# Performance work log

Hardware: AMD Instinct MI355X
Metric: run time of the kernel (lower is better)

The kernel has to match this reference:

```python
import jax, jax.numpy as jnp
import numpy as np

N, E = 40000, 640000
NODE_DIM, EDGE_DIM, H = 128, 64, 8
DK = NODE_DIM // H


def setup_inputs() -> dict:
    key = jax.random.key(0)
    ks = jax.random.split(key, 12)
    s = 1.0 / np.sqrt(NODE_DIM)
    se = 1.0 / np.sqrt(EDGE_DIM)
    return {
        "nodes": jax.random.normal(ks[0], (N, NODE_DIM), jnp.float32),
        "edge_index": jax.random.randint(ks[1], (2, E), 0, N, jnp.int64),
        "edge_attr": jax.random.normal(ks[2], (E, EDGE_DIM), jnp.float32),
        # Linear weights stored as [in, out] so y = x @ W + b
        "wq": jax.random.uniform(ks[3], (NODE_DIM, NODE_DIM), jnp.float32, -s, s),
        "bq": jnp.zeros((NODE_DIM,), jnp.float32),
        "wk": jax.random.uniform(ks[4], (NODE_DIM, NODE_DIM), jnp.float32, -s, s),
        "bk": jnp.zeros((NODE_DIM,), jnp.float32),
        "wv": jax.random.uniform(ks[5], (NODE_DIM, NODE_DIM), jnp.float32, -s, s),
        "bv": jnp.zeros((NODE_DIM,), jnp.float32),
        "we": jax.random.uniform(ks[6], (EDGE_DIM, NODE_DIM), jnp.float32, -se, se),
        "be": jnp.zeros((NODE_DIM,), jnp.float32),
        "wo": jax.random.uniform(ks[7], (NODE_DIM, NODE_DIM), jnp.float32, -s, s),
        "bo": jnp.zeros((NODE_DIM,), jnp.float32),
    }


def reference(nodes, edge_index, edge_attr, wq, bq, wk, bk, wv, bv, we, be, wo, bo):
    n = nodes.shape[0]
    inv_sqrt_dk = 1.0 / np.sqrt(DK).astype(np.float32)
    Q = (nodes @ wq + bq).reshape(n, H, DK)
    K = (nodes @ wk + bk).reshape(n, H, DK)
    V = (nodes @ wv + bv).reshape(n, H, DK)
    row, col = edge_index[0], edge_index[1]
    Qr = Q[row]                                   # [E, H, DK]
    scores = (Qr * K[col]).sum(-1) * inv_sqrt_dk  # [E, H]
    ef = (edge_attr @ we + be).reshape(-1, H, DK)
    scores = scores + (Qr * ef).sum(-1) * inv_sqrt_dk
    es = jnp.exp(scores)                          # unnormalized exp (matches torch code: no max-subtraction)
    denom = jax.ops.segment_sum(es, row, num_segments=n)       # [N, H]
    w = es / (denom[row] + 1e-8)                  # [E, H]
    msg = w[..., None] * V[col]                   # [E, H, DK]
    out = jax.ops.segment_sum(msg, row, num_segments=n).reshape(n, -1)
    return out @ wo + bo
```

## Files before the change

kernel.cpp:

```cpp
#include <hip/hip_runtime.h>
#include <hip/hip_fp16.h>

#define NN  40000
#define NE  640000
#define ND  128
#define ED  64
#define NH  8
#define DK  16
#define NWT 912

#define SCAN_NBLK 157
#define PREP_NBLK 524
#define GEMM1_NBLK 625

typedef _Float16 f16x8 __attribute__((ext_vector_type(8)));
typedef float    f32x4 __attribute__((ext_vector_type(4)));

__global__ __launch_bounds__(256) void k_prep_hist(const float* __restrict__ wq,
                                                   const float* __restrict__ bq,
                                                   const float* __restrict__ wk,
                                                   const float* __restrict__ bk,
                                                   const float* __restrict__ wv,
                                                   const float* __restrict__ bv,
                                                   const float* __restrict__ we,
                                                   const float* __restrict__ be,
                                                   const float* __restrict__ wo,
                                                   const int* __restrict__ ei,
                                                   __half* __restrict__ WT,
                                                   __half* __restrict__ woT,
                                                   float* __restrict__ bias_all,
                                                   int* __restrict__ hist) {
  if (blockIdx.x >= PREP_NBLK) {
    const int e = (blockIdx.x - PREP_NBLK) * 256 + threadIdx.x;
    if (e < NE) atomicAdd(&hist[ei[e]], 1);
    return;
  }
  int idx = blockIdx.x * 256 + threadIdx.x;
  if (idx < NWT * ND) {
    const int n = idx >> 7, k = idx & 127;
    float v;
    if (n < 128)      v = wq[k * ND + n];
    else if (n < 256) v = wk[k * ND + (n - 128)];
    else if (n < 384) v = wv[k * ND + (n - 256)];
    else if (n < 896) {
      const int col = n - 384, h = col >> 6, j = col & 63;
      const float4* a = (const float4*)(wq + (size_t)k * ND + h * DK);
      const float4* b = (const float4*)(we + (size_t)j * ND + h * DK);
      float s = 0.f;
#pragma unroll
      for (int i = 0; i < 4; ++i) {
        float4 av = a[i], bv4 = b[i];
        s = fmaf(av.x, bv4.x, s); s = fmaf(av.y, bv4.y, s);
        s = fmaf(av.z, bv4.z, s); s = fmaf(av.w, bv4.w, s);
      }
      v = 0.25f * s;
    } else if (n < 904) {
      const int h = n - 896;
      const float4* a = (const float4*)(wq + (size_t)k * ND + h * DK);
      const float4* b = (const float4*)(be + h * DK);
      float s = 0.f;
#pragma unroll
      for (int i = 0; i < 4; ++i) {
        float4 av = a[i], bv4 = b[i];
        s = fmaf(av.x, bv4.x, s); s = fmaf(av.y, bv4.y, s);
        s = fmaf(av.z, bv4.z, s); s = fmaf(av.w, bv4.w, s);
      }
      v = 0.25f * s;
    } else v = 0.f;
    WT[idx] = __float2half_rn(v);
    return;
  }
  idx -= NWT * ND;
  if (idx < ND * ND) {
    const int n = idx >> 7, k = idx & 127;
    woT[idx] = __float2half_rn(wo[k * ND + n]);
    return;
  }
  idx -= ND * ND;
  if (idx < NWT) {
    float v;
    if (idx < 128)      v = bq[idx];
    else if (idx < 256) v = bk[idx - 128];
    else if (idx < 384) v = bv[idx - 256];
    else if (idx < 896) {
      const int col = idx - 384, h = col >> 6, j = col & 63;
      const float4* a = (const float4*)(bq + h * DK);
      const float4* b = (const float4*)(we + (size_t)j * ND + h * DK);
      float s = 0.f;
#pragma unroll
      for (int i = 0; i < 4; ++i) {
        float4 av = a[i], bv4 = b[i];
        s = fmaf(av.x, bv4.x, s); s = fmaf(av.y, bv4.y, s);
        s = fmaf(av.z, bv4.z, s); s = fmaf(av.w, bv4.w, s);
      }
      v = 0.25f * s;
    } else if (idx < 904) {
      const int h = idx - 896;
      const float4* a = (const float4*)(bq + h * DK);
      const float4* b = (const float4*)(be + h * DK);
      float s = 0.f;
#pragma unroll
      for (int i = 0; i < 4; ++i) {
        float4 av = a[i], bv4 = b[i];
        s = fmaf(av.x, bv4.x, s); s = fmaf(av.y, bv4.y, s);
        s = fmaf(av.z, bv4.z, s); s = fmaf(av.w, bv4.w, s);
      }
      v = 0.25f * s;
    } else v = 0.f;
    bias_all[idx] = v;
  }
}

__global__ __launch_bounds__(256) void k_gemm1_scatter(const float* __restrict__ x,
                                                       const __half* __restrict__ WT,
                                                       const float* __restrict__ bias_all,
                                                       const int* __restrict__ ei,
                                                       int* __restrict__ cursor,
                                                       int2* __restrict__ pair,
                                                       __half* __restrict__ qh,
                                                       __half* __restrict__ K16,
                                                       __half* __restrict__ V16,
                                                       __half* __restrict__ G16,
                                                       float* __restrict__ SB) {
  __shared__ _Float16 bs[4][16][132];

  if (blockIdx.x >= GEMM1_NBLK) {
    const int e = (blockIdx.x - GEMM1_NBLK) * 256 + threadIdx.x;
    if (e < NE) {
      const int row = ei[e];
      const int col = ei[NE + e];
      const int pos = atomicAdd(&cursor[row], 1);
      pair[pos] = make_int2(col, e);
    }
    return;
  }

  const int wave = threadIdx.x >> 6;
  const int l    = threadIdx.x & 63;
  const int row  = l & 15;
  const int kq   = l >> 4;
  const int r0   = blockIdx.x * 64 + wave * 16;

  f16x8 a[4];
#pragma unroll
  for (int s = 0; s < 4; ++s) {
    const float4* ap = (const float4*)(x + (size_t)(r0 + row) * ND + s * 32 + kq * 8);
    const float4 f0 = ap[0], f1 = ap[1];
    f16x8 t;
    t[0] = (_Float16)f0.x; t[1] = (_Float16)f0.y; t[2] = (_Float16)f0.z; t[3] = (_Float16)f0.w;
    t[4] = (_Float16)f1.x; t[5] = (_Float16)f1.y; t[6] = (_Float16)f1.z; t[7] = (_Float16)f1.w;
    a[s] = t;
  }

  const int rb = r0 + kq * 4;

  for (int nc = 0; nc < 56; nc += 4) {
    __syncthreads();
    {
      const __half* src = WT + (size_t)((nc + wave) * 16 + row) * ND;
      _Float16* dst = &bs[wave][row][0];
#pragma unroll
      for (int ch = 0; ch < 4; ++ch) {
        const int o = (kq + ch * 4) * 8;
        *(f16x8*)(dst + o) = *(const f16x8*)(src + o);
      }
    }
    __syncthreads();
#pragma unroll
    for (int t = 0; t < 4; ++t) {
      const int nt = nc + t;
      f32x4 c = {0.f, 0.f, 0.f, 0.f};
#pragma unroll
      for (int s = 0; s < 4; ++s) {
        const f16x8 b = *(const f16x8*)&bs[t][row][s * 32 + kq * 8];
        c = __builtin_amdgcn_mfma_f32_16x16x32_f16(a[s], b, c, 0, 0, 0);
      }
      const int col = nt * 16 + row;
      const float bb = bias_all[col];
      if (nt < 24) {
        __half* dst = (nt < 8) ? (qh + col) : (nt < 16) ? (K16 + (col - 128)) : (V16 + (col - 256));
#pragma unroll
        for (int i = 0; i < 4; ++i)
          dst[(size_t)(rb + i) * ND] = __float2half_rn(c[i] + bb);
      } else {
        const int gcol = col - 384;
#pragma unroll
        for (int i = 0; i < 4; ++i)
          G16[(size_t)(rb + i) * 512 + gcol] = __float2half_rn(c[i] + bb);
      }
    }
  }

  {
    f32x4 c = {0.f, 0.f, 0.f, 0.f};
#pragma unroll
    for (int s = 0; s < 4; ++s) {
      const f16x8 b = *(const f16x8*)(WT + (size_t)(896 + row) * ND + s * 32 + kq * 8);
      c = __builtin_amdgcn_mfma_f32_16x16x32_f16(a[s], b, c, 0, 0, 0);
    }
    if (row < 8) {
      const float bb = bias_all[896 + row];
#pragma unroll
      for (int i = 0; i < 4; ++i)
        SB[(size_t)(rb + i) * NH + row] = c[i] + bb;
    }
  }
}

__global__ __launch_bounds__(256) void k_gemm2(const __half* __restrict__ mh,
                                               const __half* __restrict__ woT,
                                               const float* __restrict__ bo,
                                               float* __restrict__ out) {
  __shared__ _Float16 ws[128][132];
  const int tid  = threadIdx.x;
  const int wave = tid >> 6;
  const int l    = tid & 63;
  const int row  = l & 15;
  const int kq   = l >> 4;
  const int r0   = blockIdx.x * 64 + wave * 16;

  {
    const int r = tid & 127, hf = tid >> 7;
    const __half* src = woT + (size_t)r * ND + hf * 64;
    _Float16* dst = &ws[r][hf * 64];
#pragma unroll
    for (int ch = 0; ch < 8; ++ch)
      *(f16x8*)(dst + ch * 8) = *(const f16x8*)(src + ch * 8);
  }

  f16x8 a[4];
#pragma unroll
  for (int s = 0; s < 4; ++s)
    a[s] = *(const f16x8*)(mh + (size_t)(r0 + row) * ND + s * 32 + kq * 8);

  __syncthreads();

  const int rb = r0 + kq * 4;
#pragma unroll 2
  for (int nt = 0; nt < 8; ++nt) {
    f32x4 c = {0.f, 0.f, 0.f, 0.f};
#pragma unroll
    for (int s = 0; s < 4; ++s) {
      const f16x8 b = *(const f16x8*)&ws[nt * 16 + row][s * 32 + kq * 8];
      c = __builtin_amdgcn_mfma_f32_16x16x32_f16(a[s], b, c, 0, 0, 0);
    }
    const int col = nt * 16 + row;
    const float bb = bo[col];
#pragma unroll
    for (int i = 0; i < 4; ++i)
      out[(size_t)(rb + i) * ND + col] = c[i] + bb;
  }
}

__global__ __launch_bounds__(256) void k_scan1(const int* __restrict__ hist,
                                               int* __restrict__ off,
                                               int* __restrict__ bsum) {
  __shared__ int sh[256];
  const int tid = threadIdx.x;
  const int idx = blockIdx.x * 256 + tid;
  int v = (idx < NN) ? hist[idx] : 0;
  sh[tid] = v;
  __syncthreads();
#pragma unroll
  for (int d = 1; d < 256; d <<= 1) {
    int t = (tid >= d) ? sh[tid - d] : 0;
    __syncthreads();
    sh[tid] += t;
    __syncthreads();
  }
  if (idx < NN) off[idx] = sh[tid] - v;
  if (tid == 255) bsum[blockIdx.x] = sh[255];
}

__global__ __launch_bounds__(256) void k_scan2(int* __restrict__ bsum) {
  __shared__ int sh[256];
  const int tid = threadIdx.x;
  int v = (tid < SCAN_NBLK) ? bsum[tid] : 0;
  sh[tid] = v;
  __syncthreads();
#pragma unroll
  for (int d = 1; d < 256; d <<= 1) {
    int t = (tid >= d) ? sh[tid - d] : 0;
    __syncthreads();
    sh[tid] += t;
    __syncthreads();
  }
  if (tid < SCAN_NBLK) bsum[tid] = sh[tid] - v;
}

__global__ __launch_bounds__(256) void k_scan3(int* __restrict__ off,
                                               const int* __restrict__ bsum,
                                               int* __restrict__ cursor) {
  const int idx = blockIdx.x * 256 + threadIdx.x;
  if (idx < NN) {
    int o = off[idx] + bsum[blockIdx.x];
    off[idx] = o;
    cursor[idx] = o;
  }
  if (blockIdx.x == 0 && threadIdx.x == 0) off[NN] = NE;
}

__global__ __launch_bounds__(256) void k_gather(const __half* __restrict__ qh,
                                                const __half* __restrict__ K16,
                                                const __half* __restrict__ V16,
                                                const float* __restrict__ ea,
                                                const int* __restrict__ off,
                                                const int2* __restrict__ pair,
                                                const __half* __restrict__ G16,
                                                const float* __restrict__ SB,
                                                __half* __restrict__ mh) {
  __shared__ float eas[8][8 * ED];
  const int g = threadIdx.x >> 5;
  const int n = blockIdx.x * 8 + g;
  const int l = threadIdx.x & 31;
  const int h = l >> 2;
  const int q = l & 3;

  float gg[16];
  float4 qv;
  {
    const __half2* qp2 = (const __half2*)(qh + (size_t)n * ND + h * DK + q * 4);
    float2 q01 = __half22float2(qp2[0]);
    float2 q23 = __half22float2(qp2[1]);
    qv.x = q01.x * 0.25f; qv.y = q01.y * 0.25f;
    qv.z = q23.x * 0.25f; qv.w = q23.y * 0.25f;
  }
  const float sb = SB[n * NH + h];
  {
    const float4* gp = (const float4*)(G16 + (size_t)n * 512 + h * 64 + q * 16);
    float4 c0 = gp[0], c1 = gp[1];
    const __half2* h0 = (const __half2*)&c0;
    const __half2* h1 = (const __half2*)&c1;
#pragma unroll
    for (int i = 0; i < 4; ++i) {
      float2 f0 = __half22float2(h0[i]);
      gg[2 * i + 0] = f0.x; gg[2 * i + 1] = f0.y;
      float2 f1 = __half22float2(h1[i]);
      gg[8 + 2 * i + 0] = f1.x; gg[8 + 2 * i + 1] = f1.y;
    }
  }

  float4 acc = make_float4(0.f, 0.f, 0.f, 0.f);
  float den = 0.f;

  const int j0 = off[n], j1 = off[n + 1];
  const int jlast = j1 - 1;
  const int hq = h * DK + q * 4;
  const int l8 = l & 7;
  const int se = l >> 2;
  const int sp = l & 3;

  if (j0 < j1) {
    int2 p = pair[min(j0 + l8, jlast)];
    float4 er0, er1, er2, er3;
    {
      const int eid = __shfl(p.y, se, 32);
      const float4* s4 = (const float4*)(ea + (size_t)eid * ED) + sp;
      er0 = s4[0]; er1 = s4[4]; er2 = s4[8]; er3 = s4[12];
    }
    int2 pn = pair[min(j0 + 8 + l8, jlast)];

    for (int jp = j0; jp < j1; jp += 8) {
      int cols[8];
#pragma unroll
      for (int c = 0; c < 8; ++c) cols[c] = __shfl(p.x, c, 32);
      float2 kz[8], vz[8];
#pragma unroll
      for (int c = 0; c < 8; ++c) {
        kz[c] = *(const float2*)(K16 + (size_t)cols[c] * ND + hq);
        vz[c] = *(const float2*)(V16 + (size_t)cols[c] * ND + hq);
      }

      {
        float* d = &eas[g][se * ED] + sp * 4;
        *(float4*)(d + 0)  = er0; *(float4*)(d + 16) = er1;
        *(float4*)(d + 32) = er2; *(float4*)(d + 48) = er3;
      }
      int2 pf = pn;
      if (jp + 8 < j1) {
        const int eidN = __shfl(pn.y, se, 32);
        const float4* s4 = (const float4*)(ea + (size_t)eidN * ED) + sp;
        er0 = s4[0]; er1 = s4[4]; er2 = s4[8]; er3 = s4[12];
        pf = pair[min(jp + 16 + l8, jlast)];
      }

      asm volatile("s_waitcnt lgkmcnt(0)" ::: "memory");
      __builtin_amdgcn_sched_barrier(0);

      __builtin_amdgcn_s_setprio(1);
#pragma unroll
      for (int c = 0; c < 8; ++c) {
        const __half2* kh = (const __half2*)&kz[c];
        const float2 ka = __half22float2(kh[0]);
        const float2 kb = __half22float2(kh[1]);

        float s = ka.x * qv.x;
        s = fmaf(qv.y, ka.y, s); s = fmaf(qv.z, kb.x, s); s = fmaf(qv.w, kb.y, s);

        const float4* ep = (const float4*)&eas[g][c * ED + q * 16];
#pragma unroll
        for (int i = 0; i < 4; ++i) {
          float4 a = ep[i];
          s = fmaf(a.x, gg[4 * i + 0], s); s = fmaf(a.y, gg[4 * i + 1], s);
          s = fmaf(a.z, gg[4 * i + 2], s); s = fmaf(a.w, gg[4 * i + 3], s);
        }

        s += __shfl_xor(s, 1); s += __shfl_xor(s, 2);
        const float es = (jp + c < j1) ? __expf(s + sb) : 0.f;
        den += es;

        const __half2* vh = (const __half2*)&vz[c];
        const float2 va = __half22float2(vh[0]);
        const float2 vb = __half22float2(vh[1]);
        acc.x = fmaf(es, va.x, acc.x); acc.y = fmaf(es, va.y, acc.y);
        acc.z = fmaf(es, vb.x, acc.z); acc.w = fmaf(es, vb.y, acc.w);
      }
      __builtin_amdgcn_s_setprio(0);

      p = pn; pn = pf;
    }
  }

  const float inv = 1.f / (den + 1e-8f);
  union { __half2 h2[2]; float2 f; } u;
  u.h2[0] = __floats2half2_rn(acc.x * inv, acc.y * inv);
  u.h2[1] = __floats2half2_rn(acc.z * inv, acc.w * inv);
  *(float2*)(mh + (size_t)n * ND + h * DK + q * 4) = u.f;
}

extern "C" void kernel_launch(void* const* d_in, const int* in_sizes, int n_in,
                              void* d_out, int out_size, void* d_ws, size_t ws_size,
                              hipStream_t stream) {
  const float* nodes = (const float*)d_in[0];
  const int*   ei    = (const int*)d_in[1];
  const float* ea    = (const float*)d_in[2];
  const float* wq    = (const float*)d_in[3];
  const float* bq    = (const float*)d_in[4];
  const float* wk    = (const float*)d_in[5];
  const float* bk    = (const float*)d_in[6];
  const float* wv    = (const float*)d_in[7];
  const float* bv    = (const float*)d_in[8];
  const float* we    = (const float*)d_in[9];
  const float* be    = (const float*)d_in[10];
  const float* wo    = (const float*)d_in[11];
  const float* bo    = (const float*)d_in[12];
  float* out = (float*)d_out;

  const size_t NND = (size_t)NN * ND;
  __half* qh   = (__half*)d_ws;
  __half* K16  = qh + NND;
  __half* V16  = K16 + NND;
  __half* mh   = V16 + NND;
  __half* G16  = mh + NND;
  __half* WT   = G16 + (size_t)NN * 512;
  __half* woT  = WT + (size_t)NWT * ND;
  float* SB    = (float*)(woT + ND * ND);
  float* bias_all = SB + (size_t)NN * NH;
  int* hist    = (int*)(bias_all + NWT);
  int* off     = hist + NN;
  int* cursor  = off + 40004;
  int* bsum    = cursor + NN;
  int2* pair   = (int2*)(bsum + 256);

  hipMemsetAsync(hist, 0, NN * sizeof(int), stream);

  dim3 blk(256);

  k_prep_hist<<<dim3(PREP_NBLK + (NE + 255) / 256), blk, 0, stream>>>(
      wq, bq, wk, bk, wv, bv, we, be, wo, ei, WT, woT, bias_all, hist);

  k_scan1<<<dim3(SCAN_NBLK), blk, 0, stream>>>(hist, off, bsum);
  k_scan2<<<dim3(1), blk, 0, stream>>>(bsum);
  k_scan3<<<dim3(SCAN_NBLK), blk, 0, stream>>>(off, bsum, cursor);

  k_gemm1_scatter<<<dim3(GEMM1_NBLK + (NE + 255) / 256), blk, 0, stream>>>(
      nodes, WT, bias_all, ei, cursor, pair, qh, K16, V16, G16, SB);

  k_gather<<<dim3(NN / 8), blk, 0, stream>>>(qh, K16, V16, ea, off, pair, G16, SB, mh);

  k_gemm2<<<dim3(NN / 64), blk, 0, stream>>>(mh, woT, bo, out);
}
```

Baseline: 184.0 us.

## Fuse three-pass scan into one kernel and double-buffer K/V gathers

Replaces the three scan kernels with a single kernel in which each block publishes its total through a flag array and sums the totals of all earlier blocks by spinning on them. This removes two launches, relying on every block being co-resident, which holds for 157 blocks. The gather loop now prefetches the next chunk's K/V rows into a second register set while the current chunk is computed, using A/B buffer macros. This hides gather latency at the cost of more registers and possibly lower occupancy.

```diff
diff --git a/kernel.cpp b/kernel.cpp
--- a/kernel.cpp
+++ b/kernel.cpp
@@ -111,6 +111,51 @@
   }
 }
 
+__global__ __launch_bounds__(256) void k_scan_fused(const int* __restrict__ hist,
+                                                    int* __restrict__ off,
+                                                    int* __restrict__ cursor,
+                                                    int* __restrict__ pub) {
+  __shared__ int sh[256];
+  const int tid = threadIdx.x;
+  const int b = blockIdx.x;
+  const int idx = b * 256 + tid;
+  const int v = (idx < NN) ? hist[idx] : 0;
+  sh[tid] = v;
+  __syncthreads();
+#pragma unroll
+  for (int d = 1; d < 256; d <<= 1) {
+    int t = (tid >= d) ? sh[tid - d] : 0;
+    __syncthreads();
+    sh[tid] += t;
+    __syncthreads();
+  }
+  const int incl = sh[tid];
+  const int total = sh[255];
+
+  if (tid == 0) atomicExch(&pub[b], total + 1);
+
+  int contrib = 0;
+  if (tid < b) {
+    int vv;
+    do { vv = atomicAdd(&pub[tid], 0); } while (vv == 0);
+    contrib = vv - 1;
+  }
+  __syncthreads();
+  sh[tid] = contrib;
+  __syncthreads();
+#pragma unroll
+  for (int d = 128; d > 0; d >>= 1) {
+    if (tid < d) sh[tid] += sh[tid + d];
+    __syncthreads();
+  }
+  const int excl = incl - v + sh[0];
+  if (idx < NN) {
+    off[idx] = excl;
+    cursor[idx] = excl;
+  }
+  if (b == 0 && tid == 0) off[NN] = NE;
+}
+
 __global__ __launch_bounds__(256) void k_gemm1_scatter(const float* __restrict__ x,
                                                        const __half* __restrict__ WT,
                                                        const float* __restrict__ bias_all,
@@ -252,53 +297,58 @@
   }
 }
 
-__global__ __launch_bounds__(256) void k_scan1(const int* __restrict__ hist,
-                                               int* __restrict__ off,
-                                               int* __restrict__ bsum) {
-  __shared__ int sh[256];
-  const int tid = threadIdx.x;
-  const int idx = blockIdx.x * 256 + tid;
-  int v = (idx < NN) ? hist[idx] : 0;
-  sh[tid] = v;
-  __syncthreads();
-#pragma unroll
-  for (int d = 1; d < 256; d <<= 1) {
-    int t = (tid >= d) ? sh[tid - d] : 0;
-    __syncthreads();
-    sh[tid] += t;
-    __syncthreads();
-  }
-  if (idx < NN) off[idx] = sh[tid] - v;
-  if (tid == 255) bsum[blockIdx.x] = sh[255];
-}
-
-__global__ __launch_bounds__(256) void k_scan2(int* __restrict__ bsum) {
-  __shared__ int sh[256];
-  const int tid = threadIdx.x;
-  int v = (tid < SCAN_NBLK) ? bsum[tid] : 0;
-  sh[tid] = v;
-  __syncthreads();
-#pragma unroll
-  for (int d = 1; d < 256; d <<= 1) {
-    int t = (tid >= d) ? sh[tid - d] : 0;
-    __syncthreads();
-    sh[tid] += t;
-    __syncthreads();
-  }
-  if (tid < SCAN_NBLK) bsum[tid] = sh[tid] - v;
-}
-
-__global__ __launch_bounds__(256) void k_scan3(int* __restrict__ off,
-                                               const int* __restrict__ bsum,
-                                               int* __restrict__ cursor) {
-  const int idx = blockIdx.x * 256 + threadIdx.x;
-  if (idx < NN) {
-    int o = off[idx] + bsum[blockIdx.x];
-    off[idx] = o;
-    cursor[idx] = o;
-  }
-  if (blockIdx.x == 0 && threadIdx.x == 0) off[NN] = NE;
-}
+#define KVLOAD(SET, PP) do {                                                   \
+  _Pragma("unroll")                                                            \
+  for (int c = 0; c < 8; ++c) {                                                \
+    const int col = __shfl((PP).x, c, 32);                                     \
+    kz##SET[c] = *(const float2*)(K16 + (size_t)col * ND + hq);                \
+    vz##SET[c] = *(const float2*)(V16 + (size_t)col * ND + hq);                \
+  }                                                                            \
+} while (0)
+
+#define GBODY(CUR, NXT) do {                                                   \
+  {                                                        \
+    float* d = &eas[g][se * ED] + sp * 4;                                      \
+    *(float4*)(d + 0)  = er0; *(float4*)(d + 16) = er1;                        \
+    *(float4*)(d + 32) = er2; *(float4*)(d + 48) = er3;                        \
+  }                                                                            \
+  int2 pf = pn;                                                                \
+  if (jp + 8 < j1) {                                                           \
+    const int eidN = __shfl(pn.y, se, 32);                                     \
+    const float4* s4 = (const float4*)(ea + (size_t)eidN * ED) + sp;           \
+    er0 = s4[0]; er1 = s4[4]; er2 = s4[8]; er3 = s4[12];                       \
+    pf = pair[min(jp + 16 + l8, jlast)];                                       \
+    KVLOAD(NXT, pn);                                                           \
+  }                                                                            \
+  asm volatile("s_waitcnt lgkmcnt(0)" ::: "memory");                           \
+  __builtin_amdgcn_sched_barrier(0);                                           \
+  __builtin_amdgcn_s_setprio(1);                                               \
+  _Pragma("unroll")                                                            \
+  for (int c = 0; c < 8; ++c) {                                                \
+    const __half2* kh = (const __half2*)&kz##CUR[c];                           \
+    const float2 ka = __half22float2(kh[0]);                                   \
+    const float2 kb = __half22float2(kh[1]);                                   \
+    float s = ka.x * qv.x;                                                     \
+    s = fmaf(qv.y, ka.y, s); s = fmaf(qv.z, kb.x, s); s = fmaf(qv.w, kb.y, s); \
+    const float4* ep = (const float4*)&eas[g][c * ED + q * 16];                \
+    _Pragma("unroll")                                                          \
+    for (int i = 0; i < 4; ++i) {                                              \
+      float4 a = ep[i];                                                        \
+      s = fmaf(a.x, gg[4 * i + 0], s); s = fmaf(a.y, gg[4 * i + 1], s);        \
+      s = fmaf(a.z, gg[4 * i + 2], s); s = fmaf(a.w, gg[4 * i + 3], s);        \
+    }                                                                          \
+    s += __shfl_xor(s, 1); s += __shfl_xor(s, 2);                              \
+    const float es = (jp + c < j1) ? __expf(s + sb) : 0.f;                     \
+    den += es;                                                                 \
+    const __half2* vh = (const __half2*)&vz##CUR[c];                           \
+    const float2 va = __half22float2(vh[0]);                                   \
+    const float2 vb = __half22float2(vh[1]);                                   \
+    acc.x = fmaf(es, va.x, acc.x); acc.y = fmaf(es, va.y, acc.y);              \
+    acc.z = fmaf(es, vb.x, acc.z); acc.w = fmaf(es, vb.y, acc.w);              \
+  }                                                                            \
+  __builtin_amdgcn_s_setprio(0);                                               \
+  p = pn; pn = pf; jp += 8;                                                    \
+} while (0)
 
 __global__ __launch_bounds__(256) void k_gather(const __half* __restrict__ qh,
                                                 const __half* __restrict__ K16,
@@ -360,64 +410,13 @@
     }
     int2 pn = pair[min(j0 + 8 + l8, jlast)];
 
-    for (int jp = j0; jp < j1; jp += 8) {
-      int cols[8];
-#pragma unroll
-      for (int c = 0; c < 8; ++c) cols[c] = __shfl(p.x, c, 32);
-      float2 kz[8], vz[8];
-#pragma unroll
-      for (int c = 0; c < 8; ++c) {
-        kz[c] = *(const float2*)(K16 + (size_t)cols[c] * ND + hq);
-        vz[c] = *(const float2*)(V16 + (size_t)cols[c] * ND + hq);
-      }
-
-      {
-        float* d = &eas[g][se * ED] + sp * 4;
-        *(float4*)(d + 0)  = er0; *(float4*)(d + 16) = er1;
-        *(float4*)(d + 32) = er2; *(float4*)(d + 48) = er3;
-      }
-      int2 pf = pn;
-      if (jp + 8 < j1) {
-        const int eidN = __shfl(pn.y, se, 32);
-        const float4* s4 = (const float4*)(ea + (size_t)eidN * ED) + sp;
-        er0 = s4[0]; er1 = s4[4]; er2 = s4[8]; er3 = s4[12];
-        pf = pair[min(jp + 16 + l8, jlast)];
-      }
-
-      asm volatile("s_waitcnt lgkmcnt(0)" ::: "memory");
-      __builtin_amdgcn_sched_barrier(0);
-
-      __builtin_amdgcn_s_setprio(1);
-#pragma unroll
-      for (int c = 0; c < 8; ++c) {
-        const __half2* kh = (const __half2*)&kz[c];
-        const float2 ka = __half22float2(kh[0]);
-        const float2 kb = __half22float2(kh[1]);
-
-        float s = ka.x * qv.x;
-        s = fmaf(qv.y, ka.y, s); s = fmaf(qv.z, kb.x, s); s = fmaf(qv.w, kb.y, s);
-
-        const float4* ep = (const float4*)&eas[g][c * ED + q * 16];
-#pragma unroll
-        for (int i = 0; i < 4; ++i) {
-          float4 a = ep[i];
-          s = fmaf(a.x, gg[4 * i + 0], s); s = fmaf(a.y, gg[4 * i + 1], s);
-          s = fmaf(a.z, gg[4 * i + 2], s); s = fmaf(a.w, gg[4 * i + 3], s);
-        }
-
-        s += __shfl_xor(s, 1); s += __shfl_xor(s, 2);
-        const float es = (jp + c < j1) ? __expf(s + sb) : 0.f;
-        den += es;
-
-        const __half2* vh = (const __half2*)&vz[c];
-        const float2 va = __half22float2(vh[0]);
-        const float2 vb = __half22float2(vh[1]);
-        acc.x = fmaf(es, va.x, acc.x); acc.y = fmaf(es, va.y, acc.y);
-        acc.z = fmaf(es, vb.x, acc.z); acc.w = fmaf(es, vb.y, acc.w);
-      }
-      __builtin_amdgcn_s_setprio(0);
-
-      p = pn; pn = pf;
+    float2 kzA[8], vzA[8], kzB[8], vzB[8];
+    KVLOAD(A, p);
+
+    int jp = j0;
+    while (jp < j1) {
+      GBODY(A, B);
+      if (jp < j1) GBODY(B, A);
     }
   }
 
@@ -457,21 +456,19 @@
   float* SB    = (float*)(woT + ND * ND);
   float* bias_all = SB + (size_t)NN * NH;
   int* hist    = (int*)(bias_all + NWT);
-  int* off     = hist + NN;
+  int* pub     = hist + NN;
+  int* off     = pub + 160;
   int* cursor  = off + 40004;
-  int* bsum    = cursor + NN;
-  int2* pair   = (int2*)(bsum + 256);
-
-  hipMemsetAsync(hist, 0, NN * sizeof(int), stream);
+  int2* pair   = (int2*)(cursor + NN);
+
+  hipMemsetAsync(hist, 0, (NN + 160) * sizeof(int), stream);
 
   dim3 blk(256);
 
   k_prep_hist<<<dim3(PREP_NBLK + (NE + 255) / 256), blk, 0, stream>>>(
       wq, bq, wk, bk, wv, bv, we, be, wo, ei, WT, woT, bias_all, hist);
 
-  k_scan1<<<dim3(SCAN_NBLK), blk, 0, stream>>>(hist, off, bsum);
-  k_scan2<<<dim3(1), blk, 0, stream>>>(bsum);
-  k_scan3<<<dim3(SCAN_NBLK), blk, 0, stream>>>(off, bsum, cursor);
+  k_scan_fused<<<dim3(SCAN_NBLK), blk, 0, stream>>>(hist, off, cursor, pub);
 
   k_gemm1_scatter<<<dim3(GEMM1_NBLK + (NE + 255) / 256), blk, 0, stream>>>(
       nodes, WT, bias_all, ei, cursor, pair, qh, K16, V16, G16, SB);
```

New measurement: 189.2 us. +2.9%, slower.
